# Performance work log

Hardware: AMD Instinct MI355X
Metric: run time of the kernel (lower is better)

Reference implementation:

```python
import jax, jax.numpy as jnp
import numpy as np

B, LAT, ADIM, NACT, H = 131072, 64, 16, 9, 128

def setup_inputs() -> dict:
    key = jax.random.key(0)
    ks = jax.random.split(key, 24)
    p = lambda k, shp: (jax.random.normal(k, shp, dtype=jnp.float32) * 0.05)
    return {
        "z_t": jax.random.normal(ks[0], (B, LAT), dtype=jnp.float32),
        "action": jax.random.randint(ks[1], (B,), 0, NACT),
        "hidden": jnp.zeros((1, B, H), dtype=jnp.float32),
        "embed": p(ks[2], (NACT, ADIM)),
        "fuse_W": p(ks[3], (H, LAT + ADIM)), "fuse_b": p(ks[4], (H,)),
        "W_ih": p(ks[5], (3 * H, H)), "W_hh": p(ks[6], (3 * H, H)),
        "b_ih": p(ks[7], (3 * H,)), "b_hh": p(ks[8], (3 * H,)),
        "ns_W1": p(ks[9], (H, H)), "ns_b1": p(ks[10], (H,)),
        "ns_W2": p(ks[11], (LAT, H)), "ns_b2": p(ks[12], (LAT,)),
        "rw_W1": p(ks[13], (H // 2, H)), "rw_b1": p(ks[14], (H // 2,)),
        "rw_W2": p(ks[15], (1, H // 2)), "rw_b2": p(ks[16], (1,)),
        "dn_W1": p(ks[17], (H // 2, H)), "dn_b1": p(ks[18], (H // 2,)),
        "dn_W2": p(ks[19], (1, H // 2)), "dn_b2": p(ks[20], (1,)),
    }

def _mlp2(x, W1, b1, W2, b2):
    return jax.nn.relu(x @ W1.T + b1) @ W2.T + b2

def reference(z_t, action, hidden, embed, fuse_W, fuse_b, W_ih, W_hh, b_ih, b_hh,
              ns_W1, ns_b1, ns_W2, ns_b2, rw_W1, rw_b1, rw_W2, rw_b2,
              dn_W1, dn_b1, dn_W2, dn_b2):
    a_emb = embed[action]                                  # [B, ADIM]
    fused = jnp.concatenate([z_t, a_emb], axis=-1)         # [B, LAT+ADIM]
    x = jax.nn.relu(fused @ fuse_W.T + fuse_b)             # [B, H]
    h0 = hidden[0]                                         # [B, H]
    gi = x @ W_ih.T + b_ih                                 # [B, 3H]
    gh = h0 @ W_hh.T + b_hh                                # [B, 3H]
    Hd = x.shape[-1]
    r = jax.nn.sigmoid(gi[:, :Hd] + gh[:, :Hd])
    zg = jax.nn.sigmoid(gi[:, Hd:2 * Hd] + gh[:, Hd:2 * Hd])
    n = jnp.tanh(gi[:, 2 * Hd:] + r * gh[:, 2 * Hd:])
    h_new = (1.0 - zg) * n + zg * h0                       # [B, H]
    out = h_new
    z_next = _mlp2(out, ns_W1, ns_b1, ns_W2, ns_b2)        # [B, LAT]
    reward = _mlp2(out, rw_W1, rw_b1, rw_W2, rw_b2)        # [B, 1]
    done_logit = _mlp2(out, dn_W1, dn_b1, dn_W2, dn_b2)    # [B, 1]
    return (z_next, reward, done_logit, h_new[None])
```

## Files before the change

### kernel.cpp

```cpp
#include <hip/hip_runtime.h>
#include <hip/hip_bf16.h>
#include <cstddef>
#include <cstdint>

#define BATCH 131072
#define HOFF ((size_t)BATCH * 66)

typedef __attribute__((ext_vector_type(8))) short short8;
typedef __attribute__((ext_vector_type(4))) short short4v;
typedef __attribute__((ext_vector_type(4))) float f32x4;
typedef __attribute__((ext_vector_type(16))) float f32x16;

typedef const __attribute__((address_space(1))) unsigned int* gas_t;
typedef __attribute__((address_space(3))) unsigned int* las_t;

#define WS_GRU    13312
#define WS_GUNIT  26112
#define WS_HEAD   117760
#define WS_ELEMS  161280

#define G_BASE    13312
#define STR_BASE  65536

#define MFMA32(a,b,c) __builtin_amdgcn_mfma_f32_32x32x16_bf16((a),(b),(c),0,0,0)

__device__ __forceinline__ short f2bf(float x) {
    __hip_bfloat16 b = __float2bfloat16(x);
    return __builtin_bit_cast(short, b);
}
__device__ __forceinline__ float bf2f(short s) {
    unsigned u = ((unsigned)(unsigned short)s) << 16;
    return __builtin_bit_cast(float, u);
}
__device__ __forceinline__ float fsigmoid(float x) { return __builtin_amdgcn_rcpf(1.0f + __expf(-x)); }
__device__ __forceinline__ float ftanh(float x)    { return 1.0f - 2.0f * __builtin_amdgcn_rcpf(1.0f + __expf(2.0f * x)); }

__device__ __forceinline__ short8 packbf(f32x4 a, f32x4 b) {
    short8 r;
    r[0]=f2bf(a[0]); r[1]=f2bf(a[1]); r[2]=f2bf(a[2]); r[3]=f2bf(a[3]);
    r[4]=f2bf(b[0]); r[5]=f2bf(b[1]); r[6]=f2bf(b[2]); r[7]=f2bf(b[3]);
    return r;
}

template<int NCH>
__device__ __forceinline__ void stage_lds(const short* __restrict__ src, short* dst, int t) {
    constexpr int NP = (NCH + 511) / 512;
    #pragma unroll
    for (int k = 0; k < NP; ++k) {
        int c = t + 512 * k;
        if ((NCH % 512 == 0) || c < NCH)
            __builtin_amdgcn_global_load_lds((gas_t)(const void*)(src + (size_t)c * 8),
                                             (las_t)(void*)(dst + (size_t)c * 8), 16, 0, 0);
    }
}

extern "C" __global__ void prep_weights(const float* __restrict__ fuse_W,
                                        const float* __restrict__ W_ih, const float* __restrict__ W_hh,
                                        const float* __restrict__ ns_W1, const float* __restrict__ ns_W2,
                                        const float* __restrict__ rw_W1, const float* __restrict__ dn_W1,
                                        short* __restrict__ ws) {
    int i = blockIdx.x * 256 + threadIdx.x;
    if (i >= WS_ELEMS) return;
    float v = 0.f;
    if (i < WS_GRU) {
        int j = i / 104, k = i % 104;
        if (k < 80) v = fuse_W[j*80 + k];
    } else if (i < WS_HEAD) {
        int rel = i - WS_GRU;
        int u2 = rel / WS_GUNIT, e = rel % WS_GUNIT;
        int rb = e / 136, k = e % 136;
        if (k < 128) {
            int gp = rb >> 5, r = rb & 31;
            int g = gp >> 1, p = gp & 1;
            const float* W = p ? W_hh : W_ih;
            v = W[(size_t)(g*128 + u2*32 + r)*128 + k];
        }
    } else {
        int rel = i - WS_HEAD;
        int h = rel / 4352, e = rel % 4352;
        int r = e / 136, k = e % 136;
        if (k < 128) {
            const float* W; int rb;
            if (h < 4)      { W = ns_W1; rb = h*32; }
            else if (h < 6) { W = ns_W2; rb = (h-4)*32; }
            else if (h < 8) { W = rw_W1; rb = (h-6)*32; }
            else            { W = dn_W1; rb = (h-8)*32; }
            v = W[(size_t)(rb + r)*128 + k];
        }
    }
    ws[i] = f2bf(v);
}

#define GRU_J2(U, J2) do {                                                                 \
    const int ub = G_BASE + (U)*WS_GUNIT;                                                  \
    const int cb = (J2)*32 + ln;                                                           \
                                 \
    *(short8*)&S[ln*40 + hb8]      = ha[2*(J2)];                                           \
    *(short8*)&S[ln*40 + 16 + hb8] = ha[2*(J2)+1];                                         \
    unsigned h0p[8];                                                                       \
    _Pragma("unroll") for (int p = 0; p < 8; ++p) {                                        \
        const int r0 = 2*p, r1 = 2*p + 1;                                                  \
        unsigned a = (unsigned short)S[((r0&3) + 8*(r0>>2) + hr4)*40 + ln];                \
        unsigned b = (unsigned short)S[((r1&3) + 8*(r1>>2) + hr4)*40 + ln];                \
        h0p[p] = a | (b << 16);                                                            \
    }                                                                                      \
    const float br  = b_ih[cb]       + b_hh[cb];                                           \
    const float bz  = b_ih[128 + cb] + b_hh[128 + cb];                                     \
    const float bin = b_ih[256 + cb];                                                      \
    const float bhn = b_hh[256 + cb];                                                      \
    f32x16 acc, tmp;                                                                       \
                                                                  \
    acc = zz16;                                                                            \
    _Pragma("unroll") for (int kf = 0; kf < 8; ++kf) {                                     \
        const int ko = kf*16 + hb8;                                                        \
        short8 B0 = *(const short8*)&smem[ub + (0*32 + ln)*136 + ko];                      \
        acc = MFMA32(xa[kf], B0, acc);                                                     \
        short8 B1 = *(const short8*)&smem[ub + (1*32 + ln)*136 + ko];                      \
        acc = MFMA32(ha[kf], B1, acc);                                                     \
    }                                                                                      \
    _Pragma("unroll") for (int reg = 0; reg < 16; ++reg)                                   \
        tmp[reg] = fsigmoid(acc[reg] + br);                                                \
                                                                \
    acc = zz16;                                                                            \
    _Pragma("unroll") for (int kf = 0; kf < 8; ++kf) {                                     \
        short8 B5 = *(const short8*)&smem[ub + (5*32 + ln)*136 + kf*16 + hb8];             \
        acc = MFMA32(ha[kf], B5, acc);                                                     \
    }                                                                                      \
    _Pragma("unroll") for (int reg = 0; reg < 16; ++reg)                                   \
        tmp[reg] = tmp[reg] * (acc[reg] + bhn);                                            \
                                                            \
    acc = zz16;                                                                            \
    _Pragma("unroll") for (int kf = 0; kf < 8; ++kf) {                                     \
        short8 B4 = *(const short8*)&smem[ub + (4*32 + ln)*136 + kf*16 + hb8];             \
        acc = MFMA32(xa[kf], B4, acc);                                                     \
    }                                                                                      \
    _Pragma("unroll") for (int reg = 0; reg < 16; ++reg)                                   \
        tmp[reg] = ftanh(acc[reg] + bin + tmp[reg]);                                       \
                                             \
    acc = zz16;                                                                            \
    _Pragma("unroll") for (int kf = 0; kf < 8; ++kf) {                                     \
        const int ko = kf*16 + hb8;                                                        \
        short8 B2 = *(const short8*)&smem[ub + (2*32 + ln)*136 + ko];                      \
        acc = MFMA32(xa[kf], B2, acc);                                                     \
        short8 B3 = *(const short8*)&smem[ub + (3*32 + ln)*136 + ko];                      \
        acc = MFMA32(ha[kf], B3, acc);                                                     \
    }                                                                                      \
    _Pragma("unroll") for (int p = 0; p < 8; ++p) {                                        \
        unsigned hp = h0p[p];                                                              \
        _Pragma("unroll") for (int q = 0; q < 2; ++q) {                                    \
            const int reg = 2*p + q;                                                       \
            float h0v = bf2f((short)(q ? (hp >> 16) : (hp & 0xffffu)));                    \
            float zg = fsigmoid(acc[reg] + bz);                                            \
            S[((reg&3) + 8*(reg>>2) + hr4)*40 + ln] = f2bf((1.f - zg)*tmp[reg] + zg*h0v);  \
        }                                                                                  \
    }                                                                                      \
} while (0)

#define HEAD32(FRAG, BIASEXPR, HU, RELU) do {                                              \
    f32x16 a = zz16;                                                                       \
    _Pragma("unroll") for (int kf = 0; kf < 8; ++kf) {                                     \
        short8 B = *(const short8*)&smem[G_BASE + (HU)*4352 + ln*136 + kf*16 + hb8];       \
        a = MFMA32((FRAG)[kf], B, a);                                                      \
    }                                                                                      \
    const float bb = (BIASEXPR);                                                           \
    _Pragma("unroll") for (int reg = 0; reg < 16; ++reg) {                                 \
        float v = a[reg] + bb;                                                             \
        if (RELU) v = fmaxf(v, 0.f);                                                       \
        S[((reg&3) + 8*(reg>>2) + hr4)*40 + ln] = f2bf(v);                                 \
    }                                                                                      \
} while (0)

extern "C" __global__ __launch_bounds__(512, 1)
void gru_mfma(const float* __restrict__ z_t, const int* __restrict__ action,
              const float* __restrict__ hidden, const float* __restrict__ embed,
              const float* __restrict__ fuse_b,
              const float* __restrict__ b_ih, const float* __restrict__ b_hh,
              const float* __restrict__ ns_b1, const float* __restrict__ ns_b2,
              const float* __restrict__ rw_b1, const float* __restrict__ rw_W2, const float* __restrict__ rw_b2,
              const float* __restrict__ dn_b1, const float* __restrict__ dn_W2, const float* __restrict__ dn_b2,
              const short* __restrict__ ws, float* out)
{
    __shared__ __align__(16) short smem[75776];

    const int t    = threadIdx.x;
    const int lane = t & 63;
    const int w    = t >> 6;
    const int ln   = lane & 31;
    const int hb8  = (lane >> 5) * 8;
    const int hr4  = (lane >> 5) * 4;
    const int R    = blockIdx.x * 256 + w * 32;
    short* const S = &smem[STR_BASE + w * 1280];

    const f32x16 zz16 = {0,0,0,0,0,0,0,0,0,0,0,0,0,0,0,0};

    auto store_hnew = [&](int j2) {
        #pragma unroll
        for (int v = 0; v < 4; ++v) {
            int idx = v*64 + lane;
            int r = idx >> 3, c = (idx & 7) * 4;
            short4v s = *(const short4v*)&S[r*40 + c];
            f32x4 f = { bf2f(s[0]), bf2f(s[1]), bf2f(s[2]), bf2f(s[3]) };
            *(f32x4*)&out[HOFF + (size_t)(R + r)*128 + j2*32 + c] = f;
        }
    };
    auto store_z = [&](int q) {
        #pragma unroll
        for (int v = 0; v < 4; ++v) {
            int idx = v*64 + lane;
            int r = idx >> 3, c = (idx & 7) * 4;
            short4v s = *(const short4v*)&S[r*40 + c];
            f32x4 f = { bf2f(s[0]), bf2f(s[1]), bf2f(s[2]), bf2f(s[3]) };
            *(f32x4*)&out[(size_t)(R + r)*64 + q*32 + c] = f;
        }
    };
    auto hpartial = [&](const float* W2, float acc) -> float {
        int rr = lane & 31;
        #pragma unroll
        for (int kk = 0; kk < 32; kk += 8) {
            short8 s = *(const short8*)&S[rr*40 + kk];
            f32x4 w0 = *(const f32x4*)&W2[kk];
            f32x4 w1 = *(const f32x4*)&W2[kk+4];
            acc += bf2f(s[0])*w0[0] + bf2f(s[1])*w0[1] + bf2f(s[2])*w0[2] + bf2f(s[3])*w0[3]
                 + bf2f(s[4])*w1[0] + bf2f(s[5])*w1[1] + bf2f(s[6])*w1[2] + bf2f(s[7])*w1[3];
        }
        return acc;
    };

    stage_lds<1664>(ws, &smem[0], t);
    stage_lds<6528>(ws + WS_GRU, &smem[G_BASE], t);

    short8 fa[5];
    short8 ha[8];
    {
        const int row = R + ln;
        #pragma unroll
        for (int kf = 0; kf < 4; ++kf) {
            f32x4 p0 = *(const f32x4*)&z_t[(size_t)row*64 + kf*16 + hb8];
            f32x4 p1 = *(const f32x4*)&z_t[(size_t)row*64 + kf*16 + hb8 + 4];
            fa[kf] = packbf(p0, p1);
        }
        int a = action[row];
        f32x4 e0 = *(const f32x4*)&embed[a*16 + hb8];
        f32x4 e1 = *(const f32x4*)&embed[a*16 + hb8 + 4];
        fa[4] = packbf(e0, e1);
        #pragma unroll
        for (int kf = 0; kf < 8; ++kf) {
            f32x4 p0 = *(const f32x4*)&hidden[(size_t)row*128 + kf*16 + hb8];
            f32x4 p1 = *(const f32x4*)&hidden[(size_t)row*128 + kf*16 + hb8 + 4];
            ha[kf] = packbf(p0, p1);
        }
    }
    __syncthreads();

    short8 xa[8];
    #pragma unroll
    for (int n = 0; n < 4; ++n) {
        f32x16 a = zz16;
        #pragma unroll
        for (int kf = 0; kf < 5; ++kf) {
            short8 B = *(const short8*)&smem[(n*32 + ln)*104 + kf*16 + hb8];
            a = MFMA32(fa[kf], B, a);
        }
        float fb = fuse_b[n*32 + ln];
        #pragma unroll
        for (int reg = 0; reg < 16; ++reg)
            S[((reg&3) + 8*(reg>>2) + hr4)*40 + ln] = f2bf(fmaxf(a[reg] + fb, 0.f));
        xa[2*n]   = *(const short8*)&S[ln*40 + hb8];
        xa[2*n+1] = *(const short8*)&S[ln*40 + 16 + hb8];
    }

    short8 hfa[8];
    GRU_J2(0, 0);
    hfa[0] = *(const short8*)&S[ln*40 + hb8];
    hfa[1] = *(const short8*)&S[ln*40 + 16 + hb8];
    store_hnew(0);
    GRU_J2(1, 1);
    hfa[2] = *(const short8*)&S[ln*40 + hb8];
    hfa[3] = *(const short8*)&S[ln*40 + 16 + hb8];
    store_hnew(1);

    __syncthreads();
    stage_lds<6528>(ws + WS_GRU + 2*WS_GUNIT, &smem[G_BASE], t);
    __syncthreads();

    GRU_J2(0, 2);
    hfa[4] = *(const short8*)&S[ln*40 + hb8];
    hfa[5] = *(const short8*)&S[ln*40 + 16 + hb8];
    store_hnew(2);
    GRU_J2(1, 3);
    hfa[6] = *(const short8*)&S[ln*40 + hb8];
    hfa[7] = *(const short8*)&S[ln*40 + 16 + hb8];
    store_hnew(3);

    __syncthreads();
    stage_lds<5440>(ws + WS_HEAD, &smem[G_BASE], t);
    __syncthreads();

    short8 ta[8];
    HEAD32(hfa, ns_b1[ln],      0, true);
    ta[0] = *(const short8*)&S[ln*40 + hb8];
    ta[1] = *(const short8*)&S[ln*40 + 16 + hb8];
    HEAD32(hfa, ns_b1[32 + ln], 1, true);
    ta[2] = *(const short8*)&S[ln*40 + hb8];
    ta[3] = *(const short8*)&S[ln*40 + 16 + hb8];
    HEAD32(hfa, ns_b1[64 + ln], 2, true);
    ta[4] = *(const short8*)&S[ln*40 + hb8];
    ta[5] = *(const short8*)&S[ln*40 + 16 + hb8];
    HEAD32(hfa, ns_b1[96 + ln], 3, true);
    ta[6] = *(const short8*)&S[ln*40 + hb8];
    ta[7] = *(const short8*)&S[ln*40 + 16 + hb8];

    HEAD32(ta, ns_b2[ln],      4, false); store_z(0);
    HEAD32(ta, ns_b2[32 + ln], 5, false); store_z(1);

    float racc = rw_b2[0];
    HEAD32(hfa, rw_b1[ln],      6, true); racc = hpartial(rw_W2, racc);
    HEAD32(hfa, rw_b1[32 + ln], 7, true); racc = hpartial(rw_W2 + 32, racc);
    if (lane < 32) out[(size_t)BATCH*64 + R + ln] = racc;

    float dacc = dn_b2[0];
    HEAD32(hfa, dn_b1[ln],      8, true); dacc = hpartial(dn_W2, dacc);
    HEAD32(hfa, dn_b1[32 + ln], 9, true); dacc = hpartial(dn_W2 + 32, dacc);
    if (lane < 32) out[(size_t)BATCH*65 + R + ln] = dacc;
}

extern "C" void kernel_launch(void* const* d_in, const int* in_sizes, int n_in,
                              void* d_out, int out_size, void* d_ws, size_t ws_size,
                              hipStream_t stream) {
    const float* z_t    = (const float*)d_in[0];
    const int*   action = (const int*)  d_in[1];
    const float* hidden = (const float*)d_in[2];
    const float* embed  = (const float*)d_in[3];
    const float* fuse_W = (const float*)d_in[4];
    const float* fuse_b = (const float*)d_in[5];
    const float* W_ih   = (const float*)d_in[6];
    const float* W_hh   = (const float*)d_in[7];
    const float* b_ih   = (const float*)d_in[8];
    const float* b_hh   = (const float*)d_in[9];
    const float* ns_W1  = (const float*)d_in[10];
    const float* ns_b1  = (const float*)d_in[11];
    const float* ns_W2  = (const float*)d_in[12];
    const float* ns_b2  = (const float*)d_in[13];
    const float* rw_W1  = (const float*)d_in[14];
    const float* rw_b1  = (const float*)d_in[15];
    const float* rw_W2  = (const float*)d_in[16];
    const float* rw_b2  = (const float*)d_in[17];
    const float* dn_W1  = (const float*)d_in[18];
    const float* dn_b1  = (const float*)d_in[19];
    const float* dn_W2  = (const float*)d_in[20];
    const float* dn_b2  = (const float*)d_in[21];
    float* out = (float*)d_out;
    short* ws  = (short*)d_ws;

    hipLaunchKernelGGL(prep_weights, dim3((WS_ELEMS + 255) / 256), dim3(256), 0, stream,
                       fuse_W, W_ih, W_hh, ns_W1, ns_W2, rw_W1, dn_W1, ws);

    hipLaunchKernelGGL(gru_mfma, dim3(BATCH / 256), dim3(512), 0, stream,
                       z_t, action, hidden, embed,
                       fuse_b, b_ih, b_hh, ns_b1, ns_b2,
                       rw_b1, rw_W2, rw_b2, dn_b1, dn_W2, dn_b2,
                       ws, out);
}
```

Before: 78.34 us.

## Double-buffer weight slices in small LDS slots to shrink block footprint

```diff
diff --git a/kernel.cpp b/kernel.cpp
--- a/kernel.cpp
+++ b/kernel.cpp
@@ -14,13 +14,13 @@
 typedef const __attribute__((address_space(1))) unsigned int* gas_t;
 typedef __attribute__((address_space(3))) unsigned int* las_t;
 
-#define WS_GRU    13312
-#define WS_GUNIT  26112
+#define WS_G      13312
 #define WS_HEAD   117760
 #define WS_ELEMS  161280
 
-#define G_BASE    13312
-#define STR_BASE  65536
+#define SLOT_A    0
+#define SLOT_B    8704
+#define STR_BASE  17408
 
 #define MFMA32(a,b,c) __builtin_amdgcn_mfma_f32_32x32x16_bf16((a),(b),(c),0,0,0)
 
@@ -44,11 +44,11 @@
 
 template<int NCH>
 __device__ __forceinline__ void stage_lds(const short* __restrict__ src, short* dst, int t) {
-    constexpr int NP = (NCH + 511) / 512;
+    constexpr int NP = (NCH + 255) / 256;
     #pragma unroll
     for (int k = 0; k < NP; ++k) {
-        int c = t + 512 * k;
-        if ((NCH % 512 == 0) || c < NCH)
+        int c = t + 256 * k;
+        if ((NCH % 256 == 0) || c < NCH)
             __builtin_amdgcn_global_load_lds((gas_t)(const void*)(src + (size_t)c * 8),
                                              (las_t)(void*)(dst + (size_t)c * 8), 16, 0, 0);
     }
@@ -62,88 +62,91 @@
     int i = blockIdx.x * 256 + threadIdx.x;
     if (i >= WS_ELEMS) return;
     float v = 0.f;
-    if (i < WS_GRU) {
-        int j = i / 104, k = i % 104;
-        if (k < 80) v = fuse_W[j*80 + k];
+    if (i < WS_G) {
+        int half = i / 6656, e = i % 6656;
+        int r = e / 104, k = e % 104;
+        if (k < 80) v = fuse_W[(size_t)(half*64 + r)*80 + k];
     } else if (i < WS_HEAD) {
-        int rel = i - WS_GRU;
-        int u2 = rel / WS_GUNIT, e = rel % WS_GUNIT;
-        int rb = e / 136, k = e % 136;
+        int rel = i - WS_G;
+        int pidx = rel / 8704, e = rel % 8704;
+        int q = e / 4352, r = (e % 4352) / 136, k = e % 136;
         if (k < 128) {
-            int gp = rb >> 5, r = rb & 31;
-            int g = gp >> 1, p = gp & 1;
-            const float* W = p ? W_hh : W_ih;
-            v = W[(size_t)(g*128 + u2*32 + r)*128 + k];
+            int u = pidx / 3, p = pidx % 3;
+            const float* W; int gate;
+            if (p == 0)      { W = q ? W_hh : W_ih; gate = 0; }
+            else if (p == 1) { W = q ? W_ih : W_hh; gate = 2; }
+            else             { W = q ? W_hh : W_ih; gate = 1; }
+            v = W[(size_t)(gate*128 + u*32 + r)*128 + k];
         }
     } else {
         int rel = i - WS_HEAD;
-        int h = rel / 4352, e = rel % 4352;
-        int r = e / 136, k = e % 136;
+        int h = rel / 8704, e = rel % 8704;
+        int q = e / 4352, r = (e % 4352) / 136, k = e % 136;
         if (k < 128) {
             const float* W; int rb;
-            if (h < 4)      { W = ns_W1; rb = h*32; }
-            else if (h < 6) { W = ns_W2; rb = (h-4)*32; }
-            else if (h < 8) { W = rw_W1; rb = (h-6)*32; }
-            else            { W = dn_W1; rb = (h-8)*32; }
+            if (h == 0)      { W = ns_W1; rb = q*32; }
+            else if (h == 1) { W = ns_W1; rb = 64 + q*32; }
+            else if (h == 2) { W = ns_W2; rb = q*32; }
+            else if (h == 3) { W = rw_W1; rb = q*32; }
+            else             { W = dn_W1; rb = q*32; }
             v = W[(size_t)(rb + r)*128 + k];
         }
     }
     ws[i] = f2bf(v);
 }
 
-#define GRU_J2(U, J2) do {                                                                 \
-    const int ub = G_BASE + (U)*WS_GUNIT;                                                  \
-    const int cb = (J2)*32 + ln;                                                           \
-                                 \
-    *(short8*)&S[ln*40 + hb8]      = ha[2*(J2)];                                           \
-    *(short8*)&S[ln*40 + 16 + hb8] = ha[2*(J2)+1];                                         \
-    unsigned h0p[8];                                                                       \
+#define GRU_R(SB, U) do {                                                                  \
+    *(short8*)&S[ln*40 + hb8]      = ha[2*(U)];                                            \
+    *(short8*)&S[ln*40 + 16 + hb8] = ha[2*(U)+1];                                          \
     _Pragma("unroll") for (int p = 0; p < 8; ++p) {                                        \
         const int r0 = 2*p, r1 = 2*p + 1;                                                  \
         unsigned a = (unsigned short)S[((r0&3) + 8*(r0>>2) + hr4)*40 + ln];                \
         unsigned b = (unsigned short)S[((r1&3) + 8*(r1>>2) + hr4)*40 + ln];                \
         h0p[p] = a | (b << 16);                                                            \
     }                                                                                      \
-    const float br  = b_ih[cb]       + b_hh[cb];                                           \
-    const float bz  = b_ih[128 + cb] + b_hh[128 + cb];                                     \
-    const float bin = b_ih[256 + cb];                                                      \
-    const float bhn = b_hh[256 + cb];                                                      \
-    f32x16 acc, tmp;                                                                       \
-                                                                  \
+    const int cb = (U)*32 + ln;                                                            \
+    const float br = b_ih[cb] + b_hh[cb];                                                  \
+    f32x16 acc = zz16;                                                                     \
+    _Pragma("unroll") for (int kf = 0; kf < 8; ++kf) {                                     \
+        const int ko = kf*16 + hb8;                                                        \
+        short8 B0 = *(const short8*)&smem[(SB) + ln*136 + ko];                             \
+        acc = MFMA32(xa[kf], B0, acc);                                                     \
+        short8 B1 = *(const short8*)&smem[(SB) + (32 + ln)*136 + ko];                      \
+        acc = MFMA32(ha[kf], B1, acc);                                                     \
+    }                                                                                      \
+    _Pragma("unroll") for (int reg = 0; reg < 16; ++reg)                                   \
+        tmp[reg] = fsigmoid(acc[reg] + br);                                                \
+} while (0)
+
+#define GRU_N(SB, U) do {                                                                  \
+    const int cb = (U)*32 + ln;                                                            \
+    const float bin = b_ih[256 + cb], bhn = b_hh[256 + cb];                                \
+    f32x16 acc = zz16;                                                                     \
+    _Pragma("unroll") for (int kf = 0; kf < 8; ++kf) {                                     \
+        short8 B = *(const short8*)&smem[(SB) + ln*136 + kf*16 + hb8];                     \
+        acc = MFMA32(ha[kf], B, acc);                                                      \
+    }                                                                                      \
+    _Pragma("unroll") for (int reg = 0; reg < 16; ++reg)                                   \
+        tmp[reg] = tmp[reg] * (acc[reg] + bhn);                                            \
     acc = zz16;                                                                            \
     _Pragma("unroll") for (int kf = 0; kf < 8; ++kf) {                                     \
-        const int ko = kf*16 + hb8;                                                        \
-        short8 B0 = *(const short8*)&smem[ub + (0*32 + ln)*136 + ko];                      \
-        acc = MFMA32(xa[kf], B0, acc);                                                     \
-        short8 B1 = *(const short8*)&smem[ub + (1*32 + ln)*136 + ko];                      \
-        acc = MFMA32(ha[kf], B1, acc);                                                     \
-    }                                                                                      \
-    _Pragma("unroll") for (int reg = 0; reg < 16; ++reg)                                   \
-        tmp[reg] = fsigmoid(acc[reg] + br);                                                \
-                                                                \
-    acc = zz16;                                                                            \
-    _Pragma("unroll") for (int kf = 0; kf < 8; ++kf) {                                     \
-        short8 B5 = *(const short8*)&smem[ub + (5*32 + ln)*136 + kf*16 + hb8];             \
-        acc = MFMA32(ha[kf], B5, acc);                                                     \
-    }                                                                                      \
-    _Pragma("unroll") for (int reg = 0; reg < 16; ++reg)                                   \
-        tmp[reg] = tmp[reg] * (acc[reg] + bhn);                                            \
-                                                            \
-    acc = zz16;                                                                            \
-    _Pragma("unroll") for (int kf = 0; kf < 8; ++kf) {                                     \
-        short8 B4 = *(const short8*)&smem[ub + (4*32 + ln)*136 + kf*16 + hb8];             \
-        acc = MFMA32(xa[kf], B4, acc);                                                     \
+        short8 B = *(const short8*)&smem[(SB) + (32 + ln)*136 + kf*16 + hb8];              \
+        acc = MFMA32(xa[kf], B, acc);                                                      \
     }                                                                                      \
     _Pragma("unroll") for (int reg = 0; reg < 16; ++reg)                                   \
         tmp[reg] = ftanh(acc[reg] + bin + tmp[reg]);                                       \
-                                             \
-    acc = zz16;                                                                            \
+} while (0)
+
+#define GRU_Z(SB, U) do {                                                                  \
+    const int cb = (U)*32 + ln;                                                            \
+    const float bz = b_ih[128 + cb] + b_hh[128 + cb];                                      \
+    f32x16 acc = zz16;                                                                     \
     _Pragma("unroll") for (int kf = 0; kf < 8; ++kf) {                                     \
         const int ko = kf*16 + hb8;                                                        \
-        short8 B2 = *(const short8*)&smem[ub + (2*32 + ln)*136 + ko];                      \
-        acc = MFMA32(xa[kf], B2, acc);                                                     \
-        short8 B3 = *(const short8*)&smem[ub + (3*32 + ln)*136 + ko];                      \
-        acc = MFMA32(ha[kf], B3, acc);                                                     \
+        short8 B0 = *(const short8*)&smem[(SB) + ln*136 + ko];                             \
+        acc = MFMA32(xa[kf], B0, acc);                                                     \
+        short8 B1 = *(const short8*)&smem[(SB) + (32 + ln)*136 + ko];                      \
+        acc = MFMA32(ha[kf], B1, acc);                                                     \
     }                                                                                      \
     _Pragma("unroll") for (int p = 0; p < 8; ++p) {                                        \
         unsigned hp = h0p[p];                                                              \
@@ -154,12 +157,15 @@
             S[((reg&3) + 8*(reg>>2) + hr4)*40 + ln] = f2bf((1.f - zg)*tmp[reg] + zg*h0v);  \
         }                                                                                  \
     }                                                                                      \
+    hfa[2*(U)]   = *(const short8*)&S[ln*40 + hb8];                                        \
+    hfa[2*(U)+1] = *(const short8*)&S[ln*40 + 16 + hb8];                                   \
+    store_hnew(U);                                                                         \
 } while (0)
 
-#define HEAD32(FRAG, BIASEXPR, HU, RELU) do {                                              \
+#define HEAD32(FRAG, BIASEXPR, SB, Q, RELU) do {                                           \
     f32x16 a = zz16;                                                                       \
     _Pragma("unroll") for (int kf = 0; kf < 8; ++kf) {                                     \
-        short8 B = *(const short8*)&smem[G_BASE + (HU)*4352 + ln*136 + kf*16 + hb8];       \
+        short8 B = *(const short8*)&smem[(SB) + (Q)*4352 + ln*136 + kf*16 + hb8];          \
         a = MFMA32((FRAG)[kf], B, a);                                                      \
     }                                                                                      \
     const float bb = (BIASEXPR);                                                           \
@@ -170,7 +176,7 @@
     }                                                                                      \
 } while (0)
 
-extern "C" __global__ __launch_bounds__(512, 1)
+extern "C" __global__ __launch_bounds__(256, 1)
 void gru_mfma(const float* __restrict__ z_t, const int* __restrict__ action,
               const float* __restrict__ hidden, const float* __restrict__ embed,
               const float* __restrict__ fuse_b,
@@ -180,7 +186,7 @@
               const float* __restrict__ dn_b1, const float* __restrict__ dn_W2, const float* __restrict__ dn_b2,
               const short* __restrict__ ws, float* out)
 {
-    __shared__ __align__(16) short smem[75776];
+    __shared__ __align__(16) short smem[22528];
 
     const int t    = threadIdx.x;
     const int lane = t & 63;
@@ -188,7 +194,7 @@
     const int ln   = lane & 31;
     const int hb8  = (lane >> 5) * 8;
     const int hr4  = (lane >> 5) * 4;
-    const int R    = blockIdx.x * 256 + w * 32;
+    const int R    = blockIdx.x * 128 + w * 32;
     short* const S = &smem[STR_BASE + w * 1280];
 
     const f32x16 zz16 = {0,0,0,0,0,0,0,0,0,0,0,0,0,0,0,0};
@@ -226,8 +232,7 @@
         return acc;
     };
 
-    stage_lds<1664>(ws, &smem[0], t);
-    stage_lds<6528>(ws + WS_GRU, &smem[G_BASE], t);
+    stage_lds<832>(ws, &smem[SLOT_A], t);
 
     short8 fa[5];
     short8 ha[8];
@@ -250,15 +255,19 @@
             ha[kf] = packbf(p0, p1);
         }
     }
-    __syncthreads();
-
-    short8 xa[8];
+
+    short8 xa[8], hfa[8];
+    f32x16 tmp;
+    unsigned h0p[8];
+
+    __syncthreads();
+    stage_lds<832>(ws + 6656, &smem[SLOT_B], t);
     #pragma unroll
-    for (int n = 0; n < 4; ++n) {
+    for (int n = 0; n < 2; ++n) {
         f32x16 a = zz16;
         #pragma unroll
         for (int kf = 0; kf < 5; ++kf) {
-            short8 B = *(const short8*)&smem[(n*32 + ln)*104 + kf*16 + hb8];
+            short8 B = *(const short8*)&smem[SLOT_A + (n*32 + ln)*104 + kf*16 + hb8];
             a = MFMA32(fa[kf], B, a);
         }
         float fb = fuse_b[n*32 + ln];
@@ -269,58 +278,102 @@
         xa[2*n+1] = *(const short8*)&S[ln*40 + 16 + hb8];
     }
 
-    short8 hfa[8];
-    GRU_J2(0, 0);
-    hfa[0] = *(const short8*)&S[ln*40 + hb8];
-    hfa[1] = *(const short8*)&S[ln*40 + 16 + hb8];
-    store_hnew(0);
-    GRU_J2(1, 1);
-    hfa[2] = *(const short8*)&S[ln*40 + hb8];
-    hfa[3] = *(const short8*)&S[ln*40 + 16 + hb8];
-    store_hnew(1);
-
-    __syncthreads();
-    stage_lds<6528>(ws + WS_GRU + 2*WS_GUNIT, &smem[G_BASE], t);
-    __syncthreads();
-
-    GRU_J2(0, 2);
-    hfa[4] = *(const short8*)&S[ln*40 + hb8];
-    hfa[5] = *(const short8*)&S[ln*40 + 16 + hb8];
-    store_hnew(2);
-    GRU_J2(1, 3);
-    hfa[6] = *(const short8*)&S[ln*40 + hb8];
-    hfa[7] = *(const short8*)&S[ln*40 + 16 + hb8];
-    store_hnew(3);
-
-    __syncthreads();
-    stage_lds<5440>(ws + WS_HEAD, &smem[G_BASE], t);
-    __syncthreads();
+    __syncthreads();
+    stage_lds<1088>(ws + WS_G + 0*8704, &smem[SLOT_A], t);
+    #pragma unroll
+    for (int n = 2; n < 4; ++n) {
+        f32x16 a = zz16;
+        #pragma unroll
+        for (int kf = 0; kf < 5; ++kf) {
+            short8 B = *(const short8*)&smem[SLOT_B + ((n-2)*32 + ln)*104 + kf*16 + hb8];
+            a = MFMA32(fa[kf], B, a);
+        }
+        float fb = fuse_b[n*32 + ln];
+        #pragma unroll
+        for (int reg = 0; reg < 16; ++reg)
+            S[((reg&3) + 8*(reg>>2) + hr4)*40 + ln] = f2bf(fmaxf(a[reg] + fb, 0.f));
+        xa[2*n]   = *(const short8*)&S[ln*40 + hb8];
+        xa[2*n+1] = *(const short8*)&S[ln*40 + 16 + hb8];
+    }
+
+    __syncthreads();
+    stage_lds<1088>(ws + WS_G + 1*8704, &smem[SLOT_B], t);
+    GRU_R(SLOT_A, 0);
+    __syncthreads();
+    stage_lds<1088>(ws + WS_G + 2*8704, &smem[SLOT_A], t);
+    GRU_N(SLOT_B, 0);
+    __syncthreads();
+    stage_lds<1088>(ws + WS_G + 3*8704, &smem[SLOT_B], t);
+    GRU_Z(SLOT_A, 0);
+    __syncthreads();
+    stage_lds<1088>(ws + WS_G + 4*8704, &smem[SLOT_A], t);
+    GRU_R(SLOT_B, 1);
+    __syncthreads();
+    stage_lds<1088>(ws + WS_G + 5*8704, &smem[SLOT_B], t);
+    GRU_N(SLOT_A, 1);
+    __syncthreads();
+    stage_lds<1088>(ws + WS_G + 6*8704, &smem[SLOT_A], t);
+    GRU_Z(SLOT_B, 1);
+    __syncthreads();
+    stage_lds<1088>(ws + WS_G + 7*8704, &smem[SLOT_B], t);
+    GRU_R(SLOT_A, 2);
+    __syncthreads();
+    stage_lds<1088>(ws + WS_G + 8*8704, &smem[SLOT_A], t);
+    GRU_N(SLOT_B, 2);
+    __syncthreads();
+    stage_lds<1088>(ws + WS_G + 9*8704, &smem[SLOT_B], t);
+    GRU_Z(SLOT_A, 2);
+    __syncthreads();
+    stage_lds<1088>(ws + WS_G + 10*8704, &smem[SLOT_A], t);
+    GRU_R(SLOT_B, 3);
+    __syncthreads();
+    stage_lds<1088>(ws + WS_G + 11*8704, &smem[SLOT_B], t);
+    GRU_N(SLOT_A, 3);
+    __syncthreads();
+    stage_lds<1088>(ws + WS_HEAD + 0*8704, &smem[SLOT_A], t);
+    GRU_Z(SLOT_B, 3);
 
     short8 ta[8];
-    HEAD32(hfa, ns_b1[ln],      0, true);
+    __syncthreads();
+    stage_lds<1088>(ws + WS_HEAD + 1*8704, &smem[SLOT_B], t);
+    HEAD32(hfa, ns_b1[ln],      SLOT_A, 0, true);
     ta[0] = *(const short8*)&S[ln*40 + hb8];
     ta[1] = *(const short8*)&S[ln*40 + 16 + hb8];
-    HEAD32(hfa, ns_b1[32 + ln], 1, true);
+    HEAD32(hfa, ns_b1[32 + ln], SLOT_A, 1, true);
     ta[2] = *(const short8*)&S[ln*40 + hb8];
     ta[3] = *(const short8*)&S[ln*40 + 16 + hb8];
-    HEAD32(hfa, ns_b1[64 + ln], 2, true);
+
+    __syncthreads();
+    stage_lds<1088>(ws + WS_HEAD + 2*8704, &smem[SLOT_A], t);
+    HEAD32(hfa, ns_b1[64 + ln], SLOT_B, 0, true);
     ta[4] = *(const short8*)&S[ln*40 + hb8];
     ta[5] = *(const short8*)&S[ln*40 + 16 + hb8];
-    HEAD32(hfa, ns_b1[96 + ln], 3, true);
+    HEAD32(hfa, ns_b1[96 + ln], SLOT_B, 1, true);
     ta[6] = *(const short8*)&S[ln*40 + hb8];
     ta[7] = *(const short8*)&S[ln*40 + 16 + hb8];
 
-    HEAD32(ta, ns_b2[ln],      4, false); store_z(0);
-    HEAD32(ta, ns_b2[32 + ln], 5, false); store_z(1);
-
+    __syncthreads();
+    stage_lds<1088>(ws + WS_HEAD + 3*8704, &smem[SLOT_B], t);
+    HEAD32(ta, ns_b2[ln],      SLOT_A, 0, false);
+    store_z(0);
+    HEAD32(ta, ns_b2[32 + ln], SLOT_A, 1, false);
+    store_z(1);
+
+    __syncthreads();
+    stage_lds<1088>(ws + WS_HEAD + 4*8704, &smem[SLOT_A], t);
     float racc = rw_b2[0];
-    HEAD32(hfa, rw_b1[ln],      6, true); racc = hpartial(rw_W2, racc);
-    HEAD32(hfa, rw_b1[32 + ln], 7, true); racc = hpartial(rw_W2 + 32, racc);
+    HEAD32(hfa, rw_b1[ln],      SLOT_B, 0, true);
+    racc = hpartial(rw_W2, racc);
+    HEAD32(hfa, rw_b1[32 + ln], SLOT_B, 1, true);
+    racc = hpartial(rw_W2 + 32, racc);
     if (lane < 32) out[(size_t)BATCH*64 + R + ln] = racc;
 
+    __syncthreads();
     float dacc = dn_b2[0];
-    HEAD32(hfa, dn_b1[ln],      8, true); dacc = hpartial(dn_W2, dacc);
-    HEAD32(hfa, dn_b1[32 + ln], 9, true); dacc = hpartial(dn_W2 + 32, dacc);
+    HEAD32(hfa, dn_b1[ln],      SLOT_A, 0, true);
+    dacc = hpartial(dn_W2, dacc);
+    HEAD32(hfa, dn_b1[32 + ln], SLOT_A, 1, true);
+    dacc = hpartial(dn_W2 + 32, dacc);
     if (lane < 32) out[(size_t)BATCH*65 + R + ln] = dacc;
 }
 
@@ -355,7 +408,7 @@
     hipLaunchKernelGGL(prep_weights, dim3((WS_ELEMS + 255) / 256), dim3(256), 0, stream,
                        fuse_W, W_ih, W_hh, ns_W1, ns_W2, rw_W1, dn_W1, ws);
 
-    hipLaunchKernelGGL(gru_mfma, dim3(BATCH / 256), dim3(512), 0, stream,
+    hipLaunchKernelGGL(gru_mfma, dim3(BATCH / 128), dim3(256), 0, stream,
                        z_t, action, hidden, embed,
                        fuse_b, b_ih, b_hh, ns_b1, ns_b2,
                        rw_b1, rw_W2, rw_b2, dn_b1, dn_W2, dn_b2,
```

Result: slower. 82.07 us (+4.8%).
